# Optimization experiments

Measured on AMD Instinct MI355X. Metric: run time of the kernel, lower is better.

The kernel has to match this reference:

```python
import jax, jax.numpy as jnp
import numpy as np

N, E, G = 50000, 1600000, 64
XDIM, HID, NF, NG, GDIM, NL = 32, 128, 128, 50, 16, 6
CUTOFF = 10.0
SHID = 64
EPS = 1e-5

_offset = jnp.linspace(0.0, CUTOFF, NG)
_coeff = -0.5 / float((CUTOFF / (NG - 1)) ** 2)


def _bn(h, g, b):
    m = h.mean(axis=0)
    v = h.var(axis=0)
    return (h - m) * jax.lax.rsqrt(v + EPS) * g + b


def setup_inputs() -> dict:
    key = jax.random.key(0)
    ks = jax.random.split(key, 48)

    def w(k, shape):
        fan = shape[-2] if len(shape) >= 2 else shape[-1]
        return (jax.random.normal(k, shape, jnp.float32) / np.sqrt(fan)).astype(jnp.float32)

    inp = {
        "x": jax.random.normal(ks[0], (N, XDIM), jnp.float32),
        "edge_index": jax.random.randint(ks[1], (2, E), 0, N, dtype=jnp.int32).astype(jnp.int64),
        "edge_attr": jax.random.normal(ks[2], (E, 3), jnp.float32),
        "batch": jnp.sort(jax.random.randint(ks[3], (N,), 0, G, dtype=jnp.int32)).astype(jnp.int64),
        "u": jax.random.normal(ks[4], (G, GDIM), jnp.float32),
        # node encoder MLP: lin -> bn -> relu -> lin
        "We1": w(ks[5], (XDIM, HID)), "be1": jnp.zeros(HID), "ge1": jnp.ones(HID), "bte1": jnp.zeros(HID),
        "We2": w(ks[6], (HID, HID)), "be2": jnp.zeros(HID),
        # 6 stacked interactions
        "Wf1": w(ks[7], (NL, NG, NF)), "bf1": jnp.zeros((NL, NF)),
        "Wf2": w(ks[8], (NL, NF, NF)), "bf2": jnp.zeros((NL, NF)),
        "Wd1": w(ks[9], (NL, HID, HID)), "bd1": jnp.zeros((NL, HID)),
        "Wd2": w(ks[10], (NL, HID, HID)), "bd2": jnp.zeros((NL, HID)),
        # global MLP: lin -> bn -> relu -> lin
        "Wg1": w(ks[11], (GDIM, HID)), "bg1": jnp.zeros(HID), "gg1": jnp.ones(HID), "btg1": jnp.zeros(HID),
        "Wg2": w(ks[12], (HID, HID)), "bg2": jnp.zeros(HID),
        # shift predictor: [2*HID, 64, 64, 1]
        "Ws1": w(ks[13], (2 * HID, SHID)), "bs1": jnp.zeros(SHID), "gs1": jnp.ones(SHID), "bts1": jnp.zeros(SHID),
        "Ws2": w(ks[14], (SHID, SHID)), "bs2": jnp.zeros(SHID), "gs2": jnp.ones(SHID), "bts2": jnp.zeros(SHID),
        "Ws3": w(ks[15], (SHID, 1)), "bs3": jnp.zeros(1),
    }
    return inp


def reference(x, edge_index, edge_attr, batch, u,
              We1, be1, ge1, bte1, We2, be2,
              Wf1, bf1, Wf2, bf2, Wd1, bd1, Wd2, bd2,
              Wg1, bg1, gg1, btg1, Wg2, bg2,
              Ws1, bs1, gs1, bts1, Ws2, bs2, gs2, bts2, Ws3, bs3):
    row = edge_index[0]  # source j
    col = edge_index[1]  # target i

    # node encoder
    h = jax.nn.relu(_bn(x @ We1 + be1, ge1, bte1)) @ We2 + be2  # [N,HID]

    # gaussian smearing of edge lengths
    d = jnp.linalg.norm(edge_attr, axis=1)  # [E]
    ea = jnp.exp(_coeff * jnp.square(d[:, None] - _offset[None, :]))  # [E,NG]

    for l in range(NL):
        W = jax.nn.relu(ea @ Wf1[l] + bf1[l]) @ Wf2[l] + bf2[l]  # [E,NF]
        msg = h[row] * W                                          # gather + elementwise
        agg = jax.ops.segment_sum(msg, col, num_segments=N)       # scatter-add
        h = h + (jax.nn.relu(agg @ Wd1[l] + bd1[l]) @ Wd2[l] + bd2[l])

    # global MLP
    u_p = jax.nn.relu(_bn(u @ Wg1 + bg1, gg1, btg1)) @ Wg2 + bg2  # [G,HID]

    # shift predictor on [h, u_p[batch]]
    s = jnp.concatenate([h, u_p[batch]], axis=1)  # [N,2*HID]
    s = jax.nn.relu(_bn(s @ Ws1 + bs1, gs1, bts1))
    s = jax.nn.relu(_bn(s @ Ws2 + bs2, gs2, bts2))
    shifts = s @ Ws3 + bs3  # [N,1]
    return shifts, h, ea, u_p
```

## Files before the change

### kernel.cpp

```cpp
#include <hip/hip_runtime.h>

#define NN 50000
#define NE 1600000
#define NGR 64
#define XD 32
#define HID 128
#define NF 128
#define NG 50
#define GD 16
#define NL 6
#define SH 64
#define EPSF 1e-5f
#define TBL 4096
#define INVSTEP 320.0f

typedef __bf16 bf16_t;
typedef bf16_t bf16x8 __attribute__((ext_vector_type(8)));
typedef float f32x4 __attribute__((ext_vector_type(4)));

__device__ __forceinline__ unsigned pack_bf2(float a, float b) {
  unsigned short ua = __builtin_bit_cast(unsigned short, (bf16_t)a);
  unsigned short ub = __builtin_bit_cast(unsigned short, (bf16_t)b);
  return (unsigned)ua | ((unsigned)ub << 16);
}
__device__ __forceinline__ float bflo(unsigned u) { return __uint_as_float(u << 16); }
__device__ __forceinline__ float bfhi(unsigned u) { return __uint_as_float(u & 0xffff0000u); }
__device__ __forceinline__ float blerp(unsigned u, float fr) {
  float w0 = bflo(u), w1 = bfhi(u);
  return fmaf(fr, w1 - w0, w0);
}

__global__ __launch_bounds__(256) void k_hist(const int* __restrict__ col,
                                              int* __restrict__ hist) {
  for (int e = blockIdx.x * 256 + threadIdx.x; e < NE; e += gridDim.x * 256)
    atomicAdd(&hist[col[e]], 1);
}

__global__ __launch_bounds__(1024) void k_scan(int* __restrict__ hist,
                                               int* __restrict__ rowptr) {
  const int tid = threadIdx.x;
  const int CH = 49;
  const int base = tid * CH;
  int s = 0;
  for (int i = 0; i < CH; ++i) {
    int idx = base + i;
    if (idx < NN) s += hist[idx];
  }
  __shared__ int part[1024];
  part[tid] = s;
  __syncthreads();
  for (int off = 1; off < 1024; off <<= 1) {
    int v = (tid >= off) ? part[tid - off] : 0;
    __syncthreads();
    part[tid] += v;
    __syncthreads();
  }
  int run = part[tid] - s;
  for (int i = 0; i < CH; ++i) {
    int idx = base + i;
    if (idx < NN) {
      int c = hist[idx];
      rowptr[idx] = run;
      hist[idx] = run;
      run += c;
    }
  }
  if (tid == 0) rowptr[NN] = NE;
}

__global__ __launch_bounds__(256) void k_scatter2(const int* __restrict__ col,
    const int* __restrict__ row, const float* __restrict__ eattr,
    int* __restrict__ cursor, uint2* __restrict__ metap) {
  for (int e = blockIdx.x * 256 + threadIdx.x; e < NE; e += gridDim.x * 256) {
    float ax = eattr[(size_t)e * 3], ay = eattr[(size_t)e * 3 + 1], az = eattr[(size_t)e * 3 + 2];
    float d = sqrtf(ax * ax + ay * ay + az * az);
    float tt = fminf(d * INVSTEP, (float)(TBL - 2) + 0.999f);
    int id = (int)tt;
    int c = col[e];
    int pos = atomicAdd(&cursor[c], 1);
    unsigned mw = ((unsigned)row[e] << 16) | ((unsigned)id << 4) | (unsigned)(c & 15);
    metap[pos] = make_uint2(mw, __float_as_uint(tt - (float)id));
  }
}

__global__ __launch_bounds__(128) void k_tabbuild3(
    const float* __restrict__ Wf1, const float* __restrict__ bf1,
    const float* __restrict__ Wf2, const float* __restrict__ bf2,
    unsigned int* __restrict__ tabp) {
  const int bid = blockIdx.x;
  const int l = bid / (TBL / 8);
  const int t0 = (bid - l * (TBL / 8)) * 8;
  const int c = threadIdx.x;
  __shared__ float g_s[9][NG];
  __shared__ float f1_s[9][NF];
  for (int i = c; i < 9 * NG; i += 128) {
    int kk = i / NG, g = i - kk * NG;
    int t = min(t0 + kk, TBL - 1);
    float d = (float)t * (1.0f / INVSTEP);
    float z = d - 0.2040816327f * (float)g;
    g_s[kk][g] = expf(-12.005f * z * z);
  }
  __syncthreads();
  const float* W1 = Wf1 + (size_t)l * NG * NF;
  float f1r[9];
#pragma unroll
  for (int kk = 0; kk < 9; ++kk) f1r[kk] = bf1[(size_t)l * NF + c];
  for (int g = 0; g < NG; ++g) {
    float w = W1[g * NF + c];
#pragma unroll
    for (int kk = 0; kk < 9; ++kk) f1r[kk] = fmaf(g_s[kk][g], w, f1r[kk]);
  }
#pragma unroll
  for (int kk = 0; kk < 9; ++kk) f1_s[kk][c] = fmaxf(f1r[kk], 0.f);
  __syncthreads();
  const float* W2 = Wf2 + (size_t)l * NF * NF;
  float outr[9];
#pragma unroll
  for (int kk = 0; kk < 9; ++kk) outr[kk] = bf2[(size_t)l * NF + c];
  for (int k = 0; k < NF; ++k) {
    float w = W2[k * NF + c];
#pragma unroll
    for (int kk = 0; kk < 9; ++kk) outr[kk] = fmaf(f1_s[kk][k], w, outr[kk]);
  }
#pragma unroll
  for (int kk = 0; kk < 8; ++kk)
    tabp[((size_t)l * TBL + t0 + kk) * NF + c] = pack_bf2(outr[kk], outr[kk + 1]);
}

__global__ __launch_bounds__(256) void k_prepw(const float* __restrict__ Wd1,
    const float* __restrict__ Wd2,
    bf16_t* __restrict__ Wd1Thi, bf16_t* __restrict__ Wd1Tlo,
    bf16_t* __restrict__ Wd2Thi, bf16_t* __restrict__ Wd2Tlo) {
  const int S1 = NL * 128 * 128;
  int idx = blockIdx.x * 256 + threadIdx.x;
  if (idx < 2 * S1) {
    int which = idx / S1;
    int jj = idx - which * S1;
    int l = jj / (128 * 128);
    int r = jj - l * (128 * 128);
    int c = r >> 7, k = r & 127;
    const float* W = (which == 0) ? Wd1 : Wd2;
    float v = W[(size_t)l * 128 * 128 + (size_t)k * 128 + c];
    bf16_t hv = (bf16_t)v;
    bf16_t lv = (bf16_t)(v - (float)hv);
    if (which == 0) { Wd1Thi[jj] = hv; Wd1Tlo[jj] = lv; }
    else            { Wd2Thi[jj] = hv; Wd2Tlo[jj] = lv; }
  }
}

__global__ __launch_bounds__(256) void k_enc1(const float* __restrict__ x,
    const float* __restrict__ We1, const float* __restrict__ be1,
    float* __restrict__ t, float* __restrict__ stats) {
  int c = threadIdx.x & 127;
  int half = threadIdx.x >> 7;
  float b = be1[c];
  float psum = 0.f, psq = 0.f;
  for (int n = blockIdx.x * 2 + half; n < NN; n += gridDim.x * 2) {
    const float* xr = x + (size_t)n * XD;
    float v = b;
#pragma unroll
    for (int k = 0; k < XD; ++k) v = fmaf(xr[k], We1[k * HID + c], v);
    t[(size_t)n * HID + c] = v;
    psum += v; psq += v * v;
  }
  __shared__ float s0[256], s1[256];
  s0[threadIdx.x] = psum; s1[threadIdx.x] = psq;
  __syncthreads();
  if (threadIdx.x < 128) {
    atomicAdd(&stats[threadIdx.x], s0[threadIdx.x] + s0[threadIdx.x + 128]);
    atomicAdd(&stats[128 + threadIdx.x], s1[threadIdx.x] + s1[threadIdx.x + 128]);
  }
}

__global__ __launch_bounds__(128) void k_bn_fin(const float* __restrict__ gamma,
    const float* __restrict__ beta, float* __restrict__ stats, int C, float invn) {
  int c = threadIdx.x;
  if (c < C) {
    float mean = stats[c] * invn;
    float var = stats[128 + c] * invn - mean * mean;
    float a = gamma[c] * rsqrtf(var + EPSF);
    stats[256 + c] = a;
    stats[384 + c] = beta[c] - mean * a;
  }
}

__global__ __launch_bounds__(128) void k_enc2(const float* __restrict__ t,
    const float* __restrict__ stats, const float* __restrict__ We2,
    const float* __restrict__ be2, float* __restrict__ h,
    unsigned int* __restrict__ hbf) {
  __shared__ float r[HID];
  int c = threadIdx.x;
  float a = stats[256 + c], b = stats[384 + c];
  float bias = be2[c];
  for (int n = blockIdx.x; n < NN; n += gridDim.x) {
    float v = fmaf(t[(size_t)n * HID + c], a, b);
    r[c] = fmaxf(v, 0.f);
    __syncthreads();
    float acc = bias;
#pragma unroll 8
    for (int k = 0; k < HID; ++k) acc = fmaf(r[k], We2[k * HID + c], acc);
    h[(size_t)n * HID + c] = acc;
    float o = __shfl_down(acc, 1);
    if ((c & 1) == 0) hbf[(size_t)n * 64 + (c >> 1)] = pack_bf2(acc, o);
    __syncthreads();
  }
}

__global__ __launch_bounds__(256) void k_smear(const float* __restrict__ eattr,
    float* __restrict__ ea) {
  int idx = blockIdx.x * 256 + threadIdx.x;
  if (idx >= NE * NG) return;
  int e = idx / NG;
  int g = idx - e * NG;
  float ax = eattr[(size_t)e * 3], ay = eattr[(size_t)e * 3 + 1], az = eattr[(size_t)e * 3 + 2];
  float d = sqrtf(ax * ax + ay * ay + az * az);
  float off = (10.0f / 49.0f) * (float)g;
  float z = d - off;
  ea[idx] = __expf(-12.005f * z * z);
}

__global__ __launch_bounds__(256) void k_layer(
    const uint2* __restrict__ metap, const int* __restrict__ rowptr,
    const float* __restrict__ hin, const unsigned int* __restrict__ hbf,
    const unsigned int* __restrict__ tabp,
    const bf16_t* __restrict__ Wd1Thi, const bf16_t* __restrict__ Wd1Tlo,
    const bf16_t* __restrict__ Wd2Thi, const bf16_t* __restrict__ Wd2Tlo,
    const float* __restrict__ bd1, const float* __restrict__ bd2,
    float* __restrict__ hout, unsigned int* __restrict__ hbfo) {
  __shared__ __align__(16) char up[8704];
  float (*agg_s)[HID] = (float(*)[HID])up;
  bf16_t (*t1hi)[136] = (bf16_t(*)[136])up;
  bf16_t (*t1lo)[136] = (bf16_t(*)[136])(up + 4352);
  __shared__ __align__(16) bf16_t ahi_s[16][136];
  __shared__ __align__(16) bf16_t alo_s[16][136];

  const int tid = threadIdx.x;
  const int lane = tid & 63;
  const int w = tid >> 6;
  const int half = lane >> 5;
  const int c0 = (lane & 31) * 4;
  const int hoff = c0 >> 1;
  const int nb = blockIdx.x * 16;
  const int eS = rowptr[nb], eE = rowptr[nb + 16];

  for (int i = tid; i < 16 * HID; i += 256) ((float*)agg_s)[i] = 0.f;
  __syncthreads();

  {
    const int Q = (eE - eS + 3) >> 2;
    int e = eS + w * Q;
    const int wE = min(e + Q, eE);

    float a0 = 0.f, a1 = 0.f, a2 = 0.f, a3 = 0.f;
    int cur = -1;

    auto flush = [&]() {
      if (cur >= 0) {
        atomicAdd(&agg_s[cur][c0], a0);
        atomicAdd(&agg_s[cur][c0 + 1], a1);
        atomicAdd(&agg_s[cur][c0 + 2], a2);
        atomicAdd(&agg_s[cur][c0 + 3], a3);
      }
    };
    auto pbody = [&](unsigned mw, float fr, const uint2& hv, const uint4& tv,
                     bool valid) {
      if (valid) {
        int dst = mw & 0xF;
        float m0 = blerp(tv.x, fr) * bflo(hv.x);
        float m1 = blerp(tv.y, fr) * bfhi(hv.x);
        float m2 = blerp(tv.z, fr) * bflo(hv.y);
        float m3 = blerp(tv.w, fr) * bfhi(hv.y);
        if (dst != cur) {
          flush();
          cur = dst; a0 = m0; a1 = m1; a2 = m2; a3 = m3;
        } else {
          a0 += m0; a1 += m1; a2 += m2; a3 += m3;
        }
      }
    };

    if (wE - e >= 4) {
      uint2 mA0 = metap[e], mB0 = metap[e + 1];
      uint2 mA1 = metap[e + 2], mB1 = metap[e + 3];
      int ep = e + 4;
      while (true) {
        unsigned mw0 = half ? mB0.x : mA0.x;
        float fr0 = __uint_as_float(half ? mB0.y : mA0.y);
        unsigned mw1 = half ? mB1.x : mA1.x;
        float fr1 = __uint_as_float(half ? mB1.y : mA1.y);
        uint2 hv0 = *(const uint2*)(hbf + (size_t)(mw0 >> 16) * 64 + hoff);
        uint4 tv0 = *(const uint4*)(tabp + (size_t)((mw0 >> 4) & 0xFFFu) * HID + c0);
        uint2 hv1 = *(const uint2*)(hbf + (size_t)(mw1 >> 16) * 64 + hoff);
        uint4 tv1 = *(const uint4*)(tabp + (size_t)((mw1 >> 4) & 0xFFFu) * HID + c0);
        const bool more = (ep + 4 <= wE);
        uint2 nA0, nB0, nA1, nB1;
        if (more) {
          nA0 = metap[ep]; nB0 = metap[ep + 1];
          nA1 = metap[ep + 2]; nB1 = metap[ep + 3];
        }
        pbody(mw0, fr0, hv0, tv0, true);
        pbody(mw1, fr1, hv1, tv1, true);
        if (!more) break;
        mA0 = nA0; mB0 = nB0; mA1 = nA1; mB1 = nB1;
        ep += 4;
      }
      e = ep;
    }
    for (; e < wE; e += 2) {
      bool v1 = (e + 1 < wE);
      uint2 mA = metap[e];
      uint2 mB = v1 ? metap[e + 1] : mA;
      unsigned mw = half ? mB.x : mA.x;
      float fr = __uint_as_float(half ? mB.y : mA.y);
      bool valid = (half == 0) || v1;
      uint2 hv = *(const uint2*)(hbf + (size_t)(mw >> 16) * 64 + hoff);
      uint4 tv = *(const uint4*)(tabp + (size_t)((mw >> 4) & 0xFFFu) * HID + c0);
      pbody(mw, fr, hv, tv, valid);
    }
    flush();
  }
  __syncthreads();

  for (int i = tid; i < 16 * 128; i += 256) {
    int r = i >> 7, k = i & 127;
    float v = agg_s[r][k];
    bf16_t hv = (bf16_t)v;
    ahi_s[r][k] = hv;
    alo_s[r][k] = (bf16_t)(v - (float)hv);
  }
  __syncthreads();

  const int lm = lane & 15;
  const int lk = lane >> 4;
  const int colb = w * 32;
  const int k0base = lk * 8;

  f32x4 acc1g[2];
  acc1g[0] = (f32x4){0.f, 0.f, 0.f, 0.f};
  acc1g[1] = (f32x4){0.f, 0.f, 0.f, 0.f};
#pragma unroll
  for (int s = 0; s < 4; ++s) {
    int k0 = s * 32 + k0base;
    bf16x8 Ahi = *(const bf16x8*)&ahi_s[lm][k0];
    bf16x8 Alo = *(const bf16x8*)&alo_s[lm][k0];
#pragma unroll
    for (int cf = 0; cf < 2; ++cf) {
      int cc = colb + cf * 16 + lm;
      bf16x8 Bh = *(const bf16x8*)(Wd1Thi + (size_t)cc * 128 + k0);
      bf16x8 Bl = *(const bf16x8*)(Wd1Tlo + (size_t)cc * 128 + k0);
      acc1g[cf] = __builtin_amdgcn_mfma_f32_16x16x32_bf16(Ahi, Bh, acc1g[cf], 0, 0, 0);
      acc1g[cf] = __builtin_amdgcn_mfma_f32_16x16x32_bf16(Ahi, Bl, acc1g[cf], 0, 0, 0);
      acc1g[cf] = __builtin_amdgcn_mfma_f32_16x16x32_bf16(Alo, Bh, acc1g[cf], 0, 0, 0);
    }
  }
#pragma unroll
  for (int cf = 0; cf < 2; ++cf) {
    int cc = colb + cf * 16 + lm;
    float bias1 = bd1[cc];
#pragma unroll
    for (int j = 0; j < 4; ++j) {
      int r = lk * 4 + j;
      float v = fmaxf(acc1g[cf][j] + bias1, 0.f);
      bf16_t hv = (bf16_t)v;
      t1hi[r][cc] = hv;
      t1lo[r][cc] = (bf16_t)(v - (float)hv);
    }
  }
  __syncthreads();

  f32x4 acc2g[2];
  acc2g[0] = (f32x4){0.f, 0.f, 0.f, 0.f};
  acc2g[1] = (f32x4){0.f, 0.f, 0.f, 0.f};
#pragma unroll
  for (int s = 0; s < 4; ++s) {
    int k0 = s * 32 + k0base;
    bf16x8 Ahi = *(const bf16x8*)&t1hi[lm][k0];
    bf16x8 Alo = *(const bf16x8*)&t1lo[lm][k0];
#pragma unroll
    for (int cf = 0; cf < 2; ++cf) {
      int cc = colb + cf * 16 + lm;
      bf16x8 Bh = *(const bf16x8*)(Wd2Thi + (size_t)cc * 128 + k0);
      bf16x8 Bl = *(const bf16x8*)(Wd2Tlo + (size_t)cc * 128 + k0);
      acc2g[cf] = __builtin_amdgcn_mfma_f32_16x16x32_bf16(Ahi, Bh, acc2g[cf], 0, 0, 0);
      acc2g[cf] = __builtin_amdgcn_mfma_f32_16x16x32_bf16(Ahi, Bl, acc2g[cf], 0, 0, 0);
      acc2g[cf] = __builtin_amdgcn_mfma_f32_16x16x32_bf16(Alo, Bh, acc2g[cf], 0, 0, 0);
    }
  }
#pragma unroll
  for (int cf = 0; cf < 2; ++cf) {
    int cc = colb + cf * 16 + lm;
    float bias2 = bd2[cc];
#pragma unroll
    for (int j = 0; j < 4; ++j) {
      int r = nb + lk * 4 + j;
      float val = hin[(size_t)r * HID + cc] + acc2g[cf][j] + bias2;
      hout[(size_t)r * HID + cc] = val;
      float o = __shfl_xor(val, 1);
      if ((lm & 1) == 0) hbfo[(size_t)r * 64 + (cc >> 1)] = pack_bf2(val, o);
    }
  }
}

__global__ __launch_bounds__(128) void k_global(const float* __restrict__ u,
    const float* __restrict__ Wg1, const float* __restrict__ bg1,
    const float* __restrict__ gg1, const float* __restrict__ btg1,
    const float* __restrict__ Wg2, const float* __restrict__ bg2,
    float* __restrict__ u_p) {
  __shared__ float t_s[NGR][HID];
  int c = threadIdx.x;
  for (int g = 0; g < NGR; ++g) {
    float v = bg1[c];
#pragma unroll
    for (int k = 0; k < GD; ++k) v = fmaf(u[(size_t)g * GD + k], Wg1[k * HID + c], v);
    t_s[g][c] = v;
  }
  float sum = 0.f, sq = 0.f;
  for (int g = 0; g < NGR; ++g) { float v = t_s[g][c]; sum += v; sq += v * v; }
  float mean = sum * (1.f / NGR);
  float var = sq * (1.f / NGR) - mean * mean;
  float a = gg1[c] * rsqrtf(var + EPSF);
  float b = btg1[c] - mean * a;
  for (int g = 0; g < NGR; ++g) t_s[g][c] = fmaxf(fmaf(t_s[g][c], a, b), 0.f);
  __syncthreads();
  for (int g = 0; g < NGR; ++g) {
    float acc = bg2[c];
#pragma unroll 8
    for (int k = 0; k < HID; ++k) acc = fmaf(t_s[g][k], Wg2[k * HID + c], acc);
    u_p[(size_t)g * HID + c] = acc;
  }
}

__global__ __launch_bounds__(256) void k_shift1(
    const float* __restrict__ h, const float* __restrict__ u_p,
    const int* __restrict__ batch, const float* __restrict__ Ws1,
    const float* __restrict__ bs1, float* __restrict__ t1, float* __restrict__ stats) {
  __shared__ float s_in[16][2 * HID];
  const int c = threadIdx.x & 63;
  const int ng = threadIdx.x >> 6;
  float psum = 0.f, psq = 0.f;
  for (int tile = blockIdx.x; tile < NN / 16; tile += gridDim.x) {
    const int nb = tile * 16;
    for (int i = threadIdx.x; i < 16 * HID; i += 256) {
      int ln = i >> 7, k = i & 127;
      s_in[ln][k] = h[(size_t)(nb + ln) * HID + k];
      s_in[ln][HID + k] = u_p[(size_t)batch[nb + ln] * HID + k];
    }
    __syncthreads();
    float acc[4];
#pragma unroll
    for (int j = 0; j < 4; ++j) acc[j] = bs1[c];
    for (int k = 0; k < 2 * HID; ++k) {
      float w = Ws1[k * SH + c];
#pragma unroll
      for (int j = 0; j < 4; ++j) acc[j] = fmaf(s_in[ng * 4 + j][k], w, acc[j]);
    }
#pragma unroll
    for (int j = 0; j < 4; ++j) {
      t1[(size_t)(nb + ng * 4 + j) * SH + c] = acc[j];
      psum += acc[j]; psq += acc[j] * acc[j];
    }
    __syncthreads();
  }
  __shared__ float rs[256], rq[256];
  rs[threadIdx.x] = psum; rq[threadIdx.x] = psq;
  __syncthreads();
  if (threadIdx.x < 64) {
    int c2 = threadIdx.x;
    atomicAdd(&stats[c2], rs[c2] + rs[c2 + 64] + rs[c2 + 128] + rs[c2 + 192]);
    atomicAdd(&stats[128 + c2], rq[c2] + rq[c2 + 64] + rq[c2 + 128] + rq[c2 + 192]);
  }
}

__global__ __launch_bounds__(256) void k_shift2(
    const float* __restrict__ t1, float* __restrict__ stats,
    const float* __restrict__ Ws2, const float* __restrict__ bs2,
    float* __restrict__ t2) {
  __shared__ float r_s[16][SH];
  const int c = threadIdx.x & 63;
  const int ng = threadIdx.x >> 6;
  float psum = 0.f, psq = 0.f;
  for (int tile = blockIdx.x; tile < NN / 16; tile += gridDim.x) {
    const int nb = tile * 16;
    for (int i = threadIdx.x; i < 16 * SH; i += 256) {
      int ln = i >> 6, k = i & 63;
      float v = fmaf(t1[(size_t)(nb + ln) * SH + k], stats[256 + k], stats[384 + k]);
      r_s[ln][k] = fmaxf(v, 0.f);
    }
    __syncthreads();
    float acc[4];
#pragma unroll
    for (int j = 0; j < 4; ++j) acc[j] = bs2[c];
    for (int k = 0; k < SH; ++k) {
      float w = Ws2[k * SH + c];
#pragma unroll
      for (int j = 0; j < 4; ++j) acc[j] = fmaf(r_s[ng * 4 + j][k], w, acc[j]);
    }
#pragma unroll
    for (int j = 0; j < 4; ++j) {
      t2[(size_t)(nb + ng * 4 + j) * SH + c] = acc[j];
      psum += acc[j]; psq += acc[j] * acc[j];
    }
    __syncthreads();
  }
  __shared__ float rs[256], rq[256];
  rs[threadIdx.x] = psum; rq[threadIdx.x] = psq;
  __syncthreads();
  if (threadIdx.x < 64) {
    int c2 = threadIdx.x;
    atomicAdd(&stats[c2], rs[c2] + rs[c2 + 64] + rs[c2 + 128] + rs[c2 + 192]);
    atomicAdd(&stats[128 + c2], rq[c2] + rq[c2 + 64] + rq[c2 + 128] + rq[c2 + 192]);
  }
}

__global__ __launch_bounds__(256) void k_shift3(
    const float* __restrict__ t2, const float* __restrict__ stats,
    const float* __restrict__ Ws3, const float* __restrict__ bs3,
    float* __restrict__ shifts) {
  int lane = threadIdx.x & 63;
  int n = blockIdx.x * 4 + (threadIdx.x >> 6);
  if (n >= NN) return;
  float a = stats[256 + lane], b = stats[384 + lane];
  float r = fmaxf(fmaf(t2[(size_t)n * SH + lane], a, b), 0.f);
  float v = r * Ws3[lane];
#pragma unroll
  for (int off = 32; off; off >>= 1) v += __shfl_down(v, off);
  if (lane == 0) shifts[n] = v + bs3[0];
}

extern "C" void kernel_launch(void* const* d_in, const int* in_sizes, int n_in,
                              void* d_out, int out_size, void* d_ws, size_t ws_size,
                              hipStream_t stream) {
  const float* x     = (const float*)d_in[0];
  const int*   ei    = (const int*)d_in[1];
  const float* eattr = (const float*)d_in[2];
  const int*   batch = (const int*)d_in[3];
  const float* u     = (const float*)d_in[4];
  const float* We1 = (const float*)d_in[5];  const float* be1 = (const float*)d_in[6];
  const float* ge1 = (const float*)d_in[7];  const float* bte1 = (const float*)d_in[8];
  const float* We2 = (const float*)d_in[9];  const float* be2 = (const float*)d_in[10];
  const float* Wf1 = (const float*)d_in[11]; const float* bf1 = (const float*)d_in[12];
  const float* Wf2 = (const float*)d_in[13]; const float* bf2 = (const float*)d_in[14];
  const float* Wd1 = (const float*)d_in[15]; const float* bd1 = (const float*)d_in[16];
  const float* Wd2 = (const float*)d_in[17]; const float* bd2 = (const float*)d_in[18];
  const float* Wg1 = (const float*)d_in[19]; const float* bg1 = (const float*)d_in[20];
  const float* gg1 = (const float*)d_in[21]; const float* btg1 = (const float*)d_in[22];
  const float* Wg2 = (const float*)d_in[23]; const float* bg2 = (const float*)d_in[24];
  const float* Ws1 = (const float*)d_in[25]; const float* bs1 = (const float*)d_in[26];
  const float* gs1 = (const float*)d_in[27]; const float* bts1 = (const float*)d_in[28];
  const float* Ws2 = (const float*)d_in[29]; const float* bs2 = (const float*)d_in[30];
  const float* gs2 = (const float*)d_in[31]; const float* bts2 = (const float*)d_in[32];
  const float* Ws3 = (const float*)d_in[33]; const float* bs3 = (const float*)d_in[34];

  float* out    = (float*)d_out;
  float* shifts = out;
  float* h      = out + NN;
  float* ea     = out + NN + NN * HID;
  float* u_p    = out + NN + NN * HID + (size_t)NE * NG;

  char* wsb = (char*)d_ws;
  size_t off = 0;
  auto alloc = [&](size_t bytes) { void* p = wsb + off; off = (off + bytes + 255) & ~(size_t)255; return p; };
  float*  stats    = (float*)alloc(512 * sizeof(float));
  int*    hist     = (int*)alloc((size_t)NN * sizeof(int));
  int*    rowptr   = (int*)alloc((size_t)(NN + 1) * sizeof(int));
  uint2*  metap    = (uint2*)alloc((size_t)NE * sizeof(uint2));
  unsigned int* tabp = (unsigned int*)alloc((size_t)NL * TBL * HID * sizeof(unsigned int));
  bf16_t* Wd1Thi   = (bf16_t*)alloc((size_t)NL * 128 * 128 * sizeof(bf16_t));
  bf16_t* Wd1Tlo   = (bf16_t*)alloc((size_t)NL * 128 * 128 * sizeof(bf16_t));
  bf16_t* Wd2Thi   = (bf16_t*)alloc((size_t)NL * 128 * 128 * sizeof(bf16_t));
  bf16_t* Wd2Tlo   = (bf16_t*)alloc((size_t)NL * 128 * 128 * sizeof(bf16_t));
  float*  hwork    = (float*)alloc((size_t)NN * HID * sizeof(float));
  unsigned int* hbfA = (unsigned int*)alloc((size_t)NN * 64 * sizeof(unsigned int));
  unsigned int* hbfB = (unsigned int*)alloc((size_t)NN * 64 * sizeof(unsigned int));
  float*  buf1     = (float*)alloc((size_t)NN * HID * sizeof(float));
  float* t1 = buf1;
  float* t2 = buf1 + (size_t)NN * SH;

  const int* row = ei;
  const int* col = ei + NE;

  hipMemsetAsync(hist, 0, (size_t)NN * sizeof(int), stream);
  k_hist<<<512, 256, 0, stream>>>(col, hist);
  k_scan<<<1, 1024, 0, stream>>>(hist, rowptr);
  k_scatter2<<<512, 256, 0, stream>>>(col, row, eattr, hist, metap);
  k_tabbuild3<<<NL * (TBL / 8), 128, 0, stream>>>(Wf1, bf1, Wf2, bf2, tabp);
  k_prepw<<<(2 * NL * 128 * 128 + 255) / 256, 256, 0, stream>>>(
      Wd1, Wd2, Wd1Thi, Wd1Tlo, Wd2Thi, Wd2Tlo);

  hipMemsetAsync(stats, 0, 256 * sizeof(float), stream);
  k_enc1<<<512, 256, 0, stream>>>(x, We1, be1, buf1, stats);
  k_bn_fin<<<1, 128, 0, stream>>>(ge1, bte1, stats, 128, 1.f / NN);
  k_enc2<<<2048, 128, 0, stream>>>(buf1, stats, We2, be2, h, hbfA);

  k_smear<<<(NE * NG + 255) / 256, 256, 0, stream>>>(eattr, ea);

  for (int l = 0; l < NL; ++l) {
    const float* hi = (l & 1) ? hwork : h;
    float*       ho = (l & 1) ? h : hwork;
    const unsigned int* bi = (l & 1) ? hbfB : hbfA;
    unsigned int*       bo = (l & 1) ? hbfA : hbfB;
    k_layer<<<NN / 16, 256, 0, stream>>>(
        metap, rowptr, hi, bi, tabp + (size_t)l * TBL * HID,
        Wd1Thi + (size_t)l * 128 * 128, Wd1Tlo + (size_t)l * 128 * 128,
        Wd2Thi + (size_t)l * 128 * 128, Wd2Tlo + (size_t)l * 128 * 128,
        bd1 + (size_t)l * HID, bd2 + (size_t)l * HID, ho, bo);
  }

  k_global<<<1, 128, 0, stream>>>(u, Wg1, bg1, gg1, btg1, Wg2, bg2, u_p);

  hipMemsetAsync(stats, 0, 256 * sizeof(float), stream);
  k_shift1<<<1024, 256, 0, stream>>>(h, u_p, batch, Ws1, bs1, t1, stats);
  k_bn_fin<<<1, 128, 0, stream>>>(gs1, bts1, stats, 64, 1.f / NN);
  hipMemsetAsync(stats, 0, 256 * sizeof(float), stream);
  k_shift2<<<1024, 256, 0, stream>>>(t1, stats, Ws2, bs2, t2);
  k_bn_fin<<<1, 128, 0, stream>>>(gs2, bts2, stats, 64, 1.f / NN);
  k_shift3<<<(NN + 3) / 4, 256, 0, stream>>>(t2, stats, Ws3, bs3, shifts);
}
```

Before: 1.752 ms.

## Process four edges per wave with eight channels per lane; pair smear outputs

```diff
diff --git a/kernel.cpp b/kernel.cpp
--- a/kernel.cpp
+++ b/kernel.cpp
@@ -209,14 +209,15 @@
 __global__ __launch_bounds__(256) void k_smear(const float* __restrict__ eattr,
     float* __restrict__ ea) {
   int idx = blockIdx.x * 256 + threadIdx.x;
-  if (idx >= NE * NG) return;
-  int e = idx / NG;
-  int g = idx - e * NG;
+  if (idx >= NE * (NG / 2)) return;
+  int e = idx / (NG / 2);
+  int g0 = (idx - e * (NG / 2)) * 2;
   float ax = eattr[(size_t)e * 3], ay = eattr[(size_t)e * 3 + 1], az = eattr[(size_t)e * 3 + 2];
   float d = sqrtf(ax * ax + ay * ay + az * az);
-  float off = (10.0f / 49.0f) * (float)g;
-  float z = d - off;
-  ea[idx] = __expf(-12.005f * z * z);
+  float z0 = d - 0.2040816327f * (float)g0;
+  float z1 = d - 0.2040816327f * (float)(g0 + 1);
+  float2 v = make_float2(__expf(-12.005f * z0 * z0), __expf(-12.005f * z1 * z1));
+  *(float2*)(ea + (size_t)e * NG + g0) = v;
 }
 
 __global__ __launch_bounds__(256) void k_layer(
@@ -237,8 +238,8 @@
   const int tid = threadIdx.x;
   const int lane = tid & 63;
   const int w = tid >> 6;
-  const int half = lane >> 5;
-  const int c0 = (lane & 31) * 4;
+  const int q = lane >> 4;
+  const int c0 = (lane & 15) * 8;
   const int hoff = c0 >> 1;
   const int nb = blockIdx.x * 16;
   const int eS = rowptr[nb], eE = rowptr[nb + 16];
@@ -252,70 +253,76 @@
     const int wE = min(e + Q, eE);
 
     float a0 = 0.f, a1 = 0.f, a2 = 0.f, a3 = 0.f;
+    float a4 = 0.f, a5 = 0.f, a6 = 0.f, a7 = 0.f;
     int cur = -1;
 
     auto flush = [&]() {
       if (cur >= 0) {
-        atomicAdd(&agg_s[cur][c0], a0);
+        atomicAdd(&agg_s[cur][c0 + 0], a0);
         atomicAdd(&agg_s[cur][c0 + 1], a1);
         atomicAdd(&agg_s[cur][c0 + 2], a2);
         atomicAdd(&agg_s[cur][c0 + 3], a3);
+        atomicAdd(&agg_s[cur][c0 + 4], a4);
+        atomicAdd(&agg_s[cur][c0 + 5], a5);
+        atomicAdd(&agg_s[cur][c0 + 6], a6);
+        atomicAdd(&agg_s[cur][c0 + 7], a7);
       }
     };
-    auto pbody = [&](unsigned mw, float fr, const uint2& hv, const uint4& tv,
-                     bool valid) {
+    auto qbody = [&](unsigned mw, float fr, const uint4& hv,
+                     const uint4& ta, const uint4& tb, bool valid) {
       if (valid) {
         int dst = mw & 0xF;
-        float m0 = blerp(tv.x, fr) * bflo(hv.x);
-        float m1 = blerp(tv.y, fr) * bfhi(hv.x);
-        float m2 = blerp(tv.z, fr) * bflo(hv.y);
-        float m3 = blerp(tv.w, fr) * bfhi(hv.y);
+        float m0 = blerp(ta.x, fr) * bflo(hv.x);
+        float m1 = blerp(ta.y, fr) * bfhi(hv.x);
+        float m2 = blerp(ta.z, fr) * bflo(hv.y);
+        float m3 = blerp(ta.w, fr) * bfhi(hv.y);
+        float m4 = blerp(tb.x, fr) * bflo(hv.z);
+        float m5 = blerp(tb.y, fr) * bfhi(hv.z);
+        float m6 = blerp(tb.z, fr) * bflo(hv.w);
+        float m7 = blerp(tb.w, fr) * bfhi(hv.w);
         if (dst != cur) {
           flush();
-          cur = dst; a0 = m0; a1 = m1; a2 = m2; a3 = m3;
+          cur = dst;
+          a0 = m0; a1 = m1; a2 = m2; a3 = m3;
+          a4 = m4; a5 = m5; a6 = m6; a7 = m7;
         } else {
           a0 += m0; a1 += m1; a2 += m2; a3 += m3;
+          a4 += m4; a5 += m5; a6 += m6; a7 += m7;
         }
       }
     };
 
     if (wE - e >= 4) {
-      uint2 mA0 = metap[e], mB0 = metap[e + 1];
-      uint2 mA1 = metap[e + 2], mB1 = metap[e + 3];
+      uint2 m = metap[e + q];
       int ep = e + 4;
       while (true) {
-        unsigned mw0 = half ? mB0.x : mA0.x;
-        float fr0 = __uint_as_float(half ? mB0.y : mA0.y);
-        unsigned mw1 = half ? mB1.x : mA1.x;
-        float fr1 = __uint_as_float(half ? mB1.y : mA1.y);
-        uint2 hv0 = *(const uint2*)(hbf + (size_t)(mw0 >> 16) * 64 + hoff);
-        uint4 tv0 = *(const uint4*)(tabp + (size_t)((mw0 >> 4) & 0xFFFu) * HID + c0);
-        uint2 hv1 = *(const uint2*)(hbf + (size_t)(mw1 >> 16) * 64 + hoff);
-        uint4 tv1 = *(const uint4*)(tabp + (size_t)((mw1 >> 4) & 0xFFFu) * HID + c0);
+        unsigned mw = m.x;
+        float fr = __uint_as_float(m.y);
+        const size_t trow = (size_t)((mw >> 4) & 0xFFFu) * HID + c0;
+        uint4 hv = *(const uint4*)(hbf + (size_t)(mw >> 16) * 64 + hoff);
+        uint4 ta = *(const uint4*)(tabp + trow);
+        uint4 tb = *(const uint4*)(tabp + trow + 4);
         const bool more = (ep + 4 <= wE);
-        uint2 nA0, nB0, nA1, nB1;
-        if (more) {
-          nA0 = metap[ep]; nB0 = metap[ep + 1];
-          nA1 = metap[ep + 2]; nB1 = metap[ep + 3];
-        }
-        pbody(mw0, fr0, hv0, tv0, true);
-        pbody(mw1, fr1, hv1, tv1, true);
+        uint2 nm;
+        if (more) nm = metap[ep + q];
+        qbody(mw, fr, hv, ta, tb, true);
         if (!more) break;
-        mA0 = nA0; mB0 = nB0; mA1 = nA1; mB1 = nB1;
+        m = nm;
         ep += 4;
       }
       e = ep;
     }
-    for (; e < wE; e += 2) {
-      bool v1 = (e + 1 < wE);
-      uint2 mA = metap[e];
-      uint2 mB = v1 ? metap[e + 1] : mA;
-      unsigned mw = half ? mB.x : mA.x;
-      float fr = __uint_as_float(half ? mB.y : mA.y);
-      bool valid = (half == 0) || v1;
-      uint2 hv = *(const uint2*)(hbf + (size_t)(mw >> 16) * 64 + hoff);
-      uint4 tv = *(const uint4*)(tabp + (size_t)((mw >> 4) & 0xFFFu) * HID + c0);
-      pbody(mw, fr, hv, tv, valid);
+    if (e < wE) {
+      int le = e + q;
+      bool valid = le < wE;
+      uint2 m = metap[valid ? le : (wE - 1)];
+      unsigned mw = m.x;
+      float fr = __uint_as_float(m.y);
+      const size_t trow = (size_t)((mw >> 4) & 0xFFFu) * HID + c0;
+      uint4 hv = *(const uint4*)(hbf + (size_t)(mw >> 16) * 64 + hoff);
+      uint4 ta = *(const uint4*)(tabp + trow);
+      uint4 tb = *(const uint4*)(tabp + trow + 4);
+      qbody(mw, fr, hv, ta, tb, valid);
     }
     flush();
   }
@@ -592,7 +599,7 @@
   k_bn_fin<<<1, 128, 0, stream>>>(ge1, bte1, stats, 128, 1.f / NN);
   k_enc2<<<2048, 128, 0, stream>>>(buf1, stats, We2, be2, h, hbfA);
 
-  k_smear<<<(NE * NG + 255) / 256, 256, 0, stream>>>(eattr, ea);
+  k_smear<<<(NE * (NG / 2) + 255) / 256, 256, 0, stream>>>(eattr, ea);
 
   for (int l = 0; l < NL; ++l) {
     const float* hi = (l & 1) ? hwork : h;
```

Result: slower. 1.986 ms (+13.4%).

## Software-pipeline gathers in layer edge loop and vectorize smear stores

Applied to the files above, without the earlier changes.

```diff
diff --git a/kernel.cpp b/kernel.cpp
--- a/kernel.cpp
+++ b/kernel.cpp
@@ -209,14 +209,15 @@
 __global__ __launch_bounds__(256) void k_smear(const float* __restrict__ eattr,
     float* __restrict__ ea) {
   int idx = blockIdx.x * 256 + threadIdx.x;
-  if (idx >= NE * NG) return;
-  int e = idx / NG;
-  int g = idx - e * NG;
+  if (idx >= NE * (NG / 2)) return;
+  int e = idx / (NG / 2);
+  int g0 = (idx - e * (NG / 2)) * 2;
   float ax = eattr[(size_t)e * 3], ay = eattr[(size_t)e * 3 + 1], az = eattr[(size_t)e * 3 + 2];
   float d = sqrtf(ax * ax + ay * ay + az * az);
-  float off = (10.0f / 49.0f) * (float)g;
-  float z = d - off;
-  ea[idx] = __expf(-12.005f * z * z);
+  float z0 = d - 0.2040816327f * (float)g0;
+  float z1 = d - 0.2040816327f * (float)(g0 + 1);
+  float2 v = make_float2(__expf(-12.005f * z0 * z0), __expf(-12.005f * z1 * z1));
+  *(float2*)(ea + (size_t)e * NG + g0) = v;
 }
 
 __global__ __launch_bounds__(256) void k_layer(
@@ -262,60 +263,59 @@
         atomicAdd(&agg_s[cur][c0 + 3], a3);
       }
     };
-    auto pbody = [&](unsigned mw, float fr, const uint2& hv, const uint4& tv,
-                     bool valid) {
-      if (valid) {
-        int dst = mw & 0xF;
-        float m0 = blerp(tv.x, fr) * bflo(hv.x);
-        float m1 = blerp(tv.y, fr) * bfhi(hv.x);
-        float m2 = blerp(tv.z, fr) * bflo(hv.y);
-        float m3 = blerp(tv.w, fr) * bfhi(hv.y);
-        if (dst != cur) {
-          flush();
-          cur = dst; a0 = m0; a1 = m1; a2 = m2; a3 = m3;
-        } else {
-          a0 += m0; a1 += m1; a2 += m2; a3 += m3;
-        }
+    auto pbody = [&](const uint2& m, const uint2& hv, const uint4& tv) {
+      float fr = __uint_as_float(m.y);
+      int dst = m.x & 0xF;
+      float m0 = blerp(tv.x, fr) * bflo(hv.x);
+      float m1 = blerp(tv.y, fr) * bfhi(hv.x);
+      float m2 = blerp(tv.z, fr) * bflo(hv.y);
+      float m3 = blerp(tv.w, fr) * bfhi(hv.y);
+      if (dst != cur) {
+        flush();
+        cur = dst; a0 = m0; a1 = m1; a2 = m2; a3 = m3;
+      } else {
+        a0 += m0; a1 += m1; a2 += m2; a3 += m3;
       }
     };
-
-    if (wE - e >= 4) {
-      uint2 mA0 = metap[e], mB0 = metap[e + 1];
-      uint2 mA1 = metap[e + 2], mB1 = metap[e + 3];
+    auto loadd = [&](const uint2& m, uint2& hv, uint4& tv) {
+      hv = *(const uint2*)(hbf + (size_t)(m.x >> 16) * 64 + hoff);
+      tv = *(const uint4*)(tabp + (size_t)((m.x >> 4) & 0xFFFu) * HID + c0);
+    };
+
+    if (wE - e >= 8) {
+      uint2 m0a = metap[e + half], m0b = metap[e + 2 + half];
+      uint2 hv0a, hv0b; uint4 tv0a, tv0b;
+      loadd(m0a, hv0a, tv0a); loadd(m0b, hv0b, tv0b);
       int ep = e + 4;
+      uint2 m1a = metap[ep + half], m1b = metap[ep + 2 + half];
       while (true) {
-        unsigned mw0 = half ? mB0.x : mA0.x;
-        float fr0 = __uint_as_float(half ? mB0.y : mA0.y);
-        unsigned mw1 = half ? mB1.x : mA1.x;
-        float fr1 = __uint_as_float(half ? mB1.y : mA1.y);
-        uint2 hv0 = *(const uint2*)(hbf + (size_t)(mw0 >> 16) * 64 + hoff);
-        uint4 tv0 = *(const uint4*)(tabp + (size_t)((mw0 >> 4) & 0xFFFu) * HID + c0);
-        uint2 hv1 = *(const uint2*)(hbf + (size_t)(mw1 >> 16) * 64 + hoff);
-        uint4 tv1 = *(const uint4*)(tabp + (size_t)((mw1 >> 4) & 0xFFFu) * HID + c0);
-        const bool more = (ep + 4 <= wE);
-        uint2 nA0, nB0, nA1, nB1;
-        if (more) {
-          nA0 = metap[ep]; nB0 = metap[ep + 1];
-          nA1 = metap[ep + 2]; nB1 = metap[ep + 3];
+        const bool more = (ep + 8 <= wE);
+        uint2 hv1a, hv1b; uint4 tv1a, tv1b;
+        loadd(m1a, hv1a, tv1a); loadd(m1b, hv1b, tv1b);
+        uint2 m2a, m2b;
+        if (more) { m2a = metap[ep + 4 + half]; m2b = metap[ep + 6 + half]; }
+        pbody(m0a, hv0a, tv0a);
+        pbody(m0b, hv0b, tv0b);
+        if (!more) {
+          pbody(m1a, hv1a, tv1a);
+          pbody(m1b, hv1b, tv1b);
+          ep += 4;
+          break;
         }
-        pbody(mw0, fr0, hv0, tv0, true);
-        pbody(mw1, fr1, hv1, tv1, true);
-        if (!more) break;
-        mA0 = nA0; mB0 = nB0; mA1 = nA1; mB1 = nB1;
+        m0a = m1a; m0b = m1b;
+        hv0a = hv1a; hv0b = hv1b; tv0a = tv1a; tv0b = tv1b;
+        m1a = m2a; m1b = m2b;
         ep += 4;
       }
       e = ep;
     }
     for (; e < wE; e += 2) {
-      bool v1 = (e + 1 < wE);
-      uint2 mA = metap[e];
-      uint2 mB = v1 ? metap[e + 1] : mA;
-      unsigned mw = half ? mB.x : mA.x;
-      float fr = __uint_as_float(half ? mB.y : mA.y);
-      bool valid = (half == 0) || v1;
-      uint2 hv = *(const uint2*)(hbf + (size_t)(mw >> 16) * 64 + hoff);
-      uint4 tv = *(const uint4*)(tabp + (size_t)((mw >> 4) & 0xFFFu) * HID + c0);
-      pbody(mw, fr, hv, tv, valid);
+      int le = e + half;
+      bool valid = le < wE;
+      uint2 m = metap[valid ? le : (wE - 1)];
+      uint2 hv; uint4 tv;
+      loadd(m, hv, tv);
+      if (valid) pbody(m, hv, tv);
     }
     flush();
   }
@@ -592,7 +592,7 @@
   k_bn_fin<<<1, 128, 0, stream>>>(ge1, bte1, stats, 128, 1.f / NN);
   k_enc2<<<2048, 128, 0, stream>>>(buf1, stats, We2, be2, h, hbfA);
 
-  k_smear<<<(NE * NG + 255) / 256, 256, 0, stream>>>(eattr, ea);
+  k_smear<<<(NE * (NG / 2) + 255) / 256, 256, 0, stream>>>(eattr, ea);
 
   for (int l = 0; l < NL; ++l) {
     const float* hi = (l & 1) ? hwork : h;
```

After: 1.721 ms. Within noise of the previous version (-1.7%).
